# Kernel tuning notes

Hardware: AMD Instinct MI355X
Metric: run time of the kernel (lower is better)

Reference implementation:

```python
import jax, jax.numpy as jnp
import numpy as np

NIN, NHID, NDECHID, NOUT = 128, 256, 512, 10
B, N = 32, 4096


def _linear_params(key, fan_in, fan_out):
    kw, kb = jax.random.split(key)
    bound = 1.0 / np.sqrt(fan_in)
    W = jax.random.uniform(kw, (fan_in, fan_out), jnp.float32, -bound, bound)
    b = jax.random.uniform(kb, (fan_out,), jnp.float32, -bound, bound)
    return W, b


def setup_inputs() -> dict:
    key = jax.random.key(0)
    ks = jax.random.split(key, 7)
    x = jax.random.normal(ks[0], (B, N, NIN), jnp.float32)
    W1, b1 = _linear_params(ks[1], NIN, NHID)
    W2, b2 = _linear_params(ks[2], NHID, NHID)
    W3, b3 = _linear_params(ks[3], NHID, NHID)
    D1, c1 = _linear_params(ks[4], NHID, NDECHID)
    D2, c2 = _linear_params(ks[5], NDECHID, NDECHID)
    D3, c3 = _linear_params(ks[6], NDECHID, NOUT)
    return {"x": x, "W1": W1, "b1": b1, "W2": W2, "b2": b2, "W3": W3, "b3": b3,
            "D1": D1, "c1": c1, "D2": D2, "c2": c2, "D3": D3, "c3": c3}


def reference(x, W1, b1, W2, b2, W3, b3, D1, c1, D2, c2, D3, c3):
    # encoder MLP: Linear-ReLU-Linear-ReLU-Linear, then extra ReLU
    h = jax.nn.relu(x @ W1 + b1)            # [B, N, nhid]
    h = jax.nn.relu(h @ W2 + b2)
    h = jax.nn.relu(h @ W3 + b3)            # fused enc output + F.relu
    # mean_{i,j}(h_i * h_j) over the set == (mean_i h)^2 elementwise (exact identity)
    m = jnp.mean(h, axis=1)                  # [B, nhid]
    p = jax.nn.relu(m * m)                   # [B, nhid]
    # decoder MLP
    d = jax.nn.relu(p @ D1 + c1)
    d = jax.nn.relu(d @ D2 + c2)
    return d @ D3 + c3                       # [B, nout]
```

## Files before the change

### kernel.cpp

```cpp
#include <hip/hip_runtime.h>
#include <hip/hip_bf16.h>
#include <stdint.h>


#define NIN   128
#define NHID  256
#define NDEC  512
#define NOUTC 10
#define BATCH 32
#define NTOK  4096
#define MTILE 64
#define NBLK  (BATCH * (NTOK / MTILE))

#define SWZ(t) (((t) & 7) << 4)

typedef short bf16x8 __attribute__((ext_vector_type(8)));
typedef float floatx4 __attribute__((ext_vector_type(4)));

__device__ __forceinline__ uint16_t f2b(float f) {
  union { uint32_t u; float f; } v; v.f = f;
  uint32_t r = v.u + 0x7FFFu + ((v.u >> 16) & 1u);
  return (uint16_t)(r >> 16);
}
__device__ __forceinline__ uint32_t pkbf(float lo, float hi) {
  __hip_bfloat162 h = __float22bfloat162_rn(float2{lo, hi});
  union { __hip_bfloat162 h; uint32_t u; } c; c.h = h;
  return c.u;
}

__global__ __launch_bounds__(256) void pack_weights(
    const float* __restrict__ W1, const float* __restrict__ W2,
    const float* __restrict__ W3, const float* __restrict__ c3,
    uint8_t* __restrict__ pW, float* __restrict__ msum,
    float* __restrict__ out) {
  int p = blockIdx.x * blockDim.x + threadIdx.x;
  if (p < BATCH * NHID) msum[p] = 0.f;
  if (p < BATCH * NOUTC) out[p] = c3[p % NOUTC];
  if (p < 32768) {
    int j = p & 7, ln = (p >> 3) & 63, rest = p >> 9;
    int kc = rest & 3, mt = rest >> 2;
    int m = mt * 16 + (ln & 15);
    int k = kc * 32 + ((ln >> 4) << 3) + j;
    ((uint16_t*)pW)[p] = f2b(W1[k * NHID + m]);
  } else {
    int p2 = p - 32768;
    const float* W = (p2 < 65536) ? W2 : W3;
    int base = (p2 < 65536) ? 65536 : 131072;
    if (p2 >= 65536) p2 -= 65536;
    int j = p2 & 7, ln = (p2 >> 3) & 63, rest = p2 >> 9;
    int kc = rest & 7, mt = rest >> 3;
    int m = mt * 16 + (ln & 15);
    int k = kc * 32 + ((ln >> 4) << 3) + j;
    int r = __builtin_amdgcn_cvt_pk_fp8_f32(W[k * NHID + m], 0.f, 0, false);
    pW[base + p2] = (uint8_t)(r & 0xFF);
  }
}

__global__ __launch_bounds__(256) void encoder(
    const float* __restrict__ x,
    const uint8_t* __restrict__ pW,
    const float* __restrict__ b1,
    const float* __restrict__ b2,
    const float* __restrict__ b3,
    float* __restrict__ msum) {
  __shared__ __align__(16) uint8_t Hs[MTILE * 256];

  const int tid  = threadIdx.x;
  const int wave = tid >> 6;
  const int lane = tid & 63;
  const int l15  = lane & 15;
  const int q    = lane >> 4;
  const int tok0  = blockIdx.x * MTILE;
  const int batch = blockIdx.x >> 6;

  const uint16_t* pW1 = (const uint16_t*)pW;
  const uint8_t*  pW2 = pW + 65536;
  const uint8_t*  pW3 = pW + 131072;

  {
    const float4* xv = (const float4*)(x + (size_t)tok0 * NIN);
#pragma unroll
    for (int i = 0; i < 4; ++i) {
      const int u = tid + i * 256;
      float4 va = xv[2 * u];
      float4 vb = xv[2 * u + 1];
      uint4 w = make_uint4(pkbf(va.x, va.y), pkbf(va.z, va.w),
                           pkbf(vb.x, vb.y), pkbf(vb.z, vb.w));
      const int row = u >> 4;
      const int cb  = (u & 15) << 4;
      *(uint4*)&Hs[row * 256 + (cb ^ SWZ(row))] = w;
    }
  }
  __syncthreads();

  floatx4 acc[4][4];

#pragma unroll
  for (int jt = 0; jt < 4; ++jt) {
    const float4 bb = *(const float4*)&b1[wave * 64 + jt * 16 + q * 4];
#pragma unroll
    for (int tt = 0; tt < 4; ++tt)
      acc[jt][tt] = (floatx4){bb.x, bb.y, bb.z, bb.w};
  }
#pragma unroll
  for (int kc = 0; kc < 4; ++kc) {
    bf16x8 a[4], b[4];
#pragma unroll
    for (int jt = 0; jt < 4; ++jt)
      a[jt] = *(const bf16x8*)(pW1 + ((((wave * 4 + jt) * 4 + kc) * 64 + lane) << 3));
#pragma unroll
    for (int tt = 0; tt < 4; ++tt) {
      const int t = tt * 16 + l15;
      b[tt] = *(const bf16x8*)&Hs[t * 256 + ((kc * 64 + q * 16) ^ SWZ(t))];
    }
#pragma unroll
    for (int jt = 0; jt < 4; ++jt)
#pragma unroll
      for (int tt = 0; tt < 4; ++tt)
        acc[jt][tt] = __builtin_amdgcn_mfma_f32_16x16x32_bf16(
            a[jt], b[tt], acc[jt][tt], 0, 0, 0);
  }
  __syncthreads();

#pragma unroll
  for (int jt = 0; jt < 4; ++jt) {
    const int j0 = wave * 64 + jt * 16 + q * 4;
#pragma unroll
    for (int tt = 0; tt < 4; ++tt) {
      const int t = tt * 16 + l15;
      float v0 = fmaxf(acc[jt][tt][0], 0.f);
      float v1 = fmaxf(acc[jt][tt][1], 0.f);
      float v2 = fmaxf(acc[jt][tt][2], 0.f);
      float v3 = fmaxf(acc[jt][tt][3], 0.f);
      int u = __builtin_amdgcn_cvt_pk_fp8_f32(v0, v1, 0, false);
      u = __builtin_amdgcn_cvt_pk_fp8_f32(v2, v3, u, true);
      *(uint32_t*)&Hs[t * 256 + (j0 ^ SWZ(t))] = (uint32_t)u;
    }
  }
  __syncthreads();

#pragma unroll
  for (int jt = 0; jt < 4; ++jt) {
    const float4 bb = *(const float4*)&b2[wave * 64 + jt * 16 + q * 4];
#pragma unroll
    for (int tt = 0; tt < 4; ++tt)
      acc[jt][tt] = (floatx4){bb.x, bb.y, bb.z, bb.w};
  }
#pragma unroll
  for (int kc = 0; kc < 8; ++kc) {
    long a[4], b[4];
#pragma unroll
    for (int jt = 0; jt < 4; ++jt)
      a[jt] = *(const long*)(pW2 + ((((wave * 4 + jt) * 8 + kc) * 64 + lane) << 3));
#pragma unroll
    for (int tt = 0; tt < 4; ++tt) {
      const int t = tt * 16 + l15;
      b[tt] = *(const long*)&Hs[t * 256 + ((kc * 32 + q * 8) ^ SWZ(t))];
    }
#pragma unroll
    for (int jt = 0; jt < 4; ++jt)
#pragma unroll
      for (int tt = 0; tt < 4; ++tt)
        acc[jt][tt] = __builtin_amdgcn_mfma_f32_16x16x32_fp8_fp8(
            a[jt], b[tt], acc[jt][tt], 0, 0, 0);
  }
  __syncthreads();

#pragma unroll
  for (int jt = 0; jt < 4; ++jt) {
    const int j0 = wave * 64 + jt * 16 + q * 4;
#pragma unroll
    for (int tt = 0; tt < 4; ++tt) {
      const int t = tt * 16 + l15;
      float v0 = fmaxf(acc[jt][tt][0], 0.f);
      float v1 = fmaxf(acc[jt][tt][1], 0.f);
      float v2 = fmaxf(acc[jt][tt][2], 0.f);
      float v3 = fmaxf(acc[jt][tt][3], 0.f);
      int u = __builtin_amdgcn_cvt_pk_fp8_f32(v0, v1, 0, false);
      u = __builtin_amdgcn_cvt_pk_fp8_f32(v2, v3, u, true);
      *(uint32_t*)&Hs[t * 256 + (j0 ^ SWZ(t))] = (uint32_t)u;
    }
  }
  __syncthreads();

#pragma unroll
  for (int jt = 0; jt < 4; ++jt) {
    const float4 bb = *(const float4*)&b3[wave * 64 + jt * 16 + q * 4];
#pragma unroll
    for (int tt = 0; tt < 4; ++tt)
      acc[jt][tt] = (floatx4){bb.x, bb.y, bb.z, bb.w};
  }
#pragma unroll
  for (int kc = 0; kc < 8; ++kc) {
    long a[4], b[4];
#pragma unroll
    for (int jt = 0; jt < 4; ++jt)
      a[jt] = *(const long*)(pW3 + ((((wave * 4 + jt) * 8 + kc) * 64 + lane) << 3));
#pragma unroll
    for (int tt = 0; tt < 4; ++tt) {
      const int t = tt * 16 + l15;
      b[tt] = *(const long*)&Hs[t * 256 + ((kc * 32 + q * 8) ^ SWZ(t))];
    }
#pragma unroll
    for (int jt = 0; jt < 4; ++jt)
#pragma unroll
      for (int tt = 0; tt < 4; ++tt)
        acc[jt][tt] = __builtin_amdgcn_mfma_f32_16x16x32_fp8_fp8(
            a[jt], b[tt], acc[jt][tt], 0, 0, 0);
  }
#pragma unroll
  for (int jt = 0; jt < 4; ++jt) {
    float s0 = 0.f, s1 = 0.f, s2 = 0.f, s3 = 0.f;
#pragma unroll
    for (int tt = 0; tt < 4; ++tt) {
      s0 += fmaxf(acc[jt][tt][0], 0.f);
      s1 += fmaxf(acc[jt][tt][1], 0.f);
      s2 += fmaxf(acc[jt][tt][2], 0.f);
      s3 += fmaxf(acc[jt][tt][3], 0.f);
    }
#pragma unroll
    for (int m = 1; m <= 8; m <<= 1) {
      s0 += __shfl_xor(s0, m);
      s1 += __shfl_xor(s1, m);
      s2 += __shfl_xor(s2, m);
      s3 += __shfl_xor(s3, m);
    }
    if (l15 == 0) {
      const int jb = batch * NHID + wave * 64 + jt * 16 + q * 4;
      atomicAdd(&msum[jb + 0], s0);
      atomicAdd(&msum[jb + 1], s1);
      atomicAdd(&msum[jb + 2], s2);
      atomicAdd(&msum[jb + 3], s3);
    }
  }
}

__global__ __launch_bounds__(1024) void decoder(
    const float* __restrict__ msum,
    const float* __restrict__ D1, const float* __restrict__ c1,
    const float* __restrict__ D2, const float* __restrict__ c2,
    const float* __restrict__ D3,
    float* __restrict__ out) {
  __shared__ float p[NHID];
  __shared__ float d1[NDEC];
  __shared__ float d2q[128];
  __shared__ __align__(16) float red[4096];
  const int b = blockIdx.x >> 2, qd = blockIdx.x & 3, t = threadIdx.x;

  if (t < NHID) {
    float m = msum[b * NHID + t] * (1.f / NTOK);
    p[t] = m * m;
  }
  __syncthreads();

  {
    const int jg = t & 127;
    const int ks = t >> 7;
    const float4* D1v = (const float4*)D1;
    float4 s = {0.f, 0.f, 0.f, 0.f};
    for (int k = ks * 32; k < ks * 32 + 32; ++k) {
      float4 w = D1v[k * 128 + jg];
      float pv = p[k];
      s.x += pv * w.x; s.y += pv * w.y; s.z += pv * w.z; s.w += pv * w.w;
    }
    *(float4*)&red[t * 4] = s;
    __syncthreads();
    if (t < NDEC) {
      float v = c1[t];
#pragma unroll
      for (int i = 0; i < 8; ++i) v += red[i * 512 + t];
      d1[t] = fmaxf(v, 0.f);
    }
    __syncthreads();
  }

  {
    const int jg2 = t & 31;
    const int ks2 = t >> 5;
    const float4* D2v = (const float4*)D2;
    float4 s = {0.f, 0.f, 0.f, 0.f};
    for (int k = ks2 * 16; k < ks2 * 16 + 16; ++k) {
      float4 w = D2v[k * 128 + qd * 32 + jg2];
      float hv = d1[k];
      s.x += hv * w.x; s.y += hv * w.y; s.z += hv * w.z; s.w += hv * w.w;
    }
    *(float4*)&red[t * 4] = s;
    __syncthreads();
    if (t < 128) {
      float v = c2[qd * 128 + t];
#pragma unroll
      for (int i = 0; i < 32; ++i) v += red[i * 128 + t];
      d2q[t] = fmaxf(v, 0.f);
    }
    __syncthreads();
  }

  {
    const int j3 = t & 15;
    const int kc = t >> 4;
    float s = 0.f;
    if (j3 < NOUTC)
      for (int k = kc * 2; k < kc * 2 + 2; ++k)
        s += d2q[k] * D3[(qd * 128 + k) * NOUTC + j3];
    red[t] = s;
    __syncthreads();
    if (t < NOUTC) {
      float v = 0.f;
#pragma unroll
      for (int i = 0; i < 64; ++i) v += red[i * 16 + t];
      atomicAdd(&out[b * NOUTC + t], v);
    }
  }
}

extern "C" void kernel_launch(void* const* d_in, const int* in_sizes, int n_in,
                              void* d_out, int out_size, void* d_ws, size_t ws_size,
                              hipStream_t stream) {
  const float* x  = (const float*)d_in[0];
  const float* W1 = (const float*)d_in[1];
  const float* b1 = (const float*)d_in[2];
  const float* W2 = (const float*)d_in[3];
  const float* b2 = (const float*)d_in[4];
  const float* W3 = (const float*)d_in[5];
  const float* b3 = (const float*)d_in[6];
  const float* D1 = (const float*)d_in[7];
  const float* c1 = (const float*)d_in[8];
  const float* D2 = (const float*)d_in[9];
  const float* c2 = (const float*)d_in[10];
  const float* D3 = (const float*)d_in[11];
  const float* c3 = (const float*)d_in[12];

  uint8_t* pW   = (uint8_t*)d_ws;
  float*   msum = (float*)((char*)d_ws + 384 * 1024);

  pack_weights<<<640, 256, 0, stream>>>(W1, W2, W3, c3, pW, msum,
                                        (float*)d_out);
  encoder<<<NBLK, 256, 0, stream>>>(x, pW, b1, b2, b3, msum);
  decoder<<<128, 1024, 0, stream>>>(msum, D1, c1, D2, c2, D3,
                                    (float*)d_out);
}
```

Before: 171.2 us.

## Split encoder tile across eight waves and stage per-block sums in LDS

The encoder block grows from 4 to 8 waves. Each wave now owns 32 output features (2 column tiles) instead of 64, which halves the accumulator registers per thread and lets more waves be resident (launch bounds 512, 8). The final per-feature sums go into a shared scratch array, and then 256 threads each issue one atomic, replacing the scattered per-lane atomics. The cost is that each B fragment read from LDS is reused by only 2 A tiles instead of 4, which raises LDS traffic per MFMA, and there is one extra barrier.

Measured after the change: 177.2 us. 1.04x slower.

```diff
diff --git a/kernel.cpp b/kernel.cpp
--- a/kernel.cpp
+++ b/kernel.cpp
@@ -56,7 +56,7 @@
   }
 }
 
-__global__ __launch_bounds__(256) void encoder(
+__global__ __launch_bounds__(512, 8) void encoder(
     const float* __restrict__ x,
     const uint8_t* __restrict__ pW,
     const float* __restrict__ b1,
@@ -64,6 +64,7 @@
     const float* __restrict__ b3,
     float* __restrict__ msum) {
   __shared__ __align__(16) uint8_t Hs[MTILE * 256];
+  __shared__ __align__(16) float scr[NHID];
 
   const int tid  = threadIdx.x;
   const int wave = tid >> 6;
@@ -80,8 +81,8 @@
   {
     const float4* xv = (const float4*)(x + (size_t)tok0 * NIN);
 #pragma unroll
-    for (int i = 0; i < 4; ++i) {
-      const int u = tid + i * 256;
+    for (int i = 0; i < 2; ++i) {
+      const int u = tid + i * 512;
       float4 va = xv[2 * u];
       float4 vb = xv[2 * u + 1];
       uint4 w = make_uint4(pkbf(va.x, va.y), pkbf(va.z, va.w),
@@ -93,38 +94,32 @@
   }
   __syncthreads();
 
-  floatx4 acc[4][4];
-
-#pragma unroll
-  for (int jt = 0; jt < 4; ++jt) {
-    const float4 bb = *(const float4*)&b1[wave * 64 + jt * 16 + q * 4];
+  floatx4 acc[2][4];
+
+#pragma unroll
+  for (int jt = 0; jt < 2; ++jt) {
+    const float4 bb = *(const float4*)&b1[(wave * 2 + jt) * 16 + q * 4];
 #pragma unroll
     for (int tt = 0; tt < 4; ++tt)
       acc[jt][tt] = (floatx4){bb.x, bb.y, bb.z, bb.w};
   }
 #pragma unroll
   for (int kc = 0; kc < 4; ++kc) {
-    bf16x8 a[4], b[4];
-#pragma unroll
-    for (int jt = 0; jt < 4; ++jt)
-      a[jt] = *(const bf16x8*)(pW1 + ((((wave * 4 + jt) * 4 + kc) * 64 + lane) << 3));
-#pragma unroll
-    for (int tt = 0; tt < 4; ++tt) {
-      const int t = tt * 16 + l15;
-      b[tt] = *(const bf16x8*)&Hs[t * 256 + ((kc * 64 + q * 16) ^ SWZ(t))];
-    }
-#pragma unroll
-    for (int jt = 0; jt < 4; ++jt)
-#pragma unroll
-      for (int tt = 0; tt < 4; ++tt)
-        acc[jt][tt] = __builtin_amdgcn_mfma_f32_16x16x32_bf16(
-            a[jt], b[tt], acc[jt][tt], 0, 0, 0);
-  }
-  __syncthreads();
-
-#pragma unroll
-  for (int jt = 0; jt < 4; ++jt) {
-    const int j0 = wave * 64 + jt * 16 + q * 4;
+    bf16x8 a0 = *(const bf16x8*)(pW1 + ((((wave * 2 + 0) * 4 + kc) * 64 + lane) << 3));
+    bf16x8 a1 = *(const bf16x8*)(pW1 + ((((wave * 2 + 1) * 4 + kc) * 64 + lane) << 3));
+#pragma unroll
+    for (int tt = 0; tt < 4; ++tt) {
+      const int t = tt * 16 + l15;
+      bf16x8 b = *(const bf16x8*)&Hs[t * 256 + ((kc * 64 + q * 16) ^ SWZ(t))];
+      acc[0][tt] = __builtin_amdgcn_mfma_f32_16x16x32_bf16(a0, b, acc[0][tt], 0, 0, 0);
+      acc[1][tt] = __builtin_amdgcn_mfma_f32_16x16x32_bf16(a1, b, acc[1][tt], 0, 0, 0);
+    }
+  }
+  __syncthreads();
+
+#pragma unroll
+  for (int jt = 0; jt < 2; ++jt) {
+    const int j0 = (wave * 2 + jt) * 16 + q * 4;
 #pragma unroll
     for (int tt = 0; tt < 4; ++tt) {
       const int t = tt * 16 + l15;
@@ -140,35 +135,29 @@
   __syncthreads();
 
 #pragma unroll
-  for (int jt = 0; jt < 4; ++jt) {
-    const float4 bb = *(const float4*)&b2[wave * 64 + jt * 16 + q * 4];
+  for (int jt = 0; jt < 2; ++jt) {
+    const float4 bb = *(const float4*)&b2[(wave * 2 + jt) * 16 + q * 4];
 #pragma unroll
     for (int tt = 0; tt < 4; ++tt)
       acc[jt][tt] = (floatx4){bb.x, bb.y, bb.z, bb.w};
   }
 #pragma unroll
   for (int kc = 0; kc < 8; ++kc) {
-    long a[4], b[4];
-#pragma unroll
-    for (int jt = 0; jt < 4; ++jt)
-      a[jt] = *(const long*)(pW2 + ((((wave * 4 + jt) * 8 + kc) * 64 + lane) << 3));
-#pragma unroll
-    for (int tt = 0; tt < 4; ++tt) {
-      const int t = tt * 16 + l15;
-      b[tt] = *(const long*)&Hs[t * 256 + ((kc * 32 + q * 8) ^ SWZ(t))];
-    }
-#pragma unroll
-    for (int jt = 0; jt < 4; ++jt)
-#pragma unroll
-      for (int tt = 0; tt < 4; ++tt)
-        acc[jt][tt] = __builtin_amdgcn_mfma_f32_16x16x32_fp8_fp8(
-            a[jt], b[tt], acc[jt][tt], 0, 0, 0);
-  }
-  __syncthreads();
-
-#pragma unroll
-  for (int jt = 0; jt < 4; ++jt) {
-    const int j0 = wave * 64 + jt * 16 + q * 4;
+    long a0 = *(const long*)(pW2 + ((((wave * 2 + 0) * 8 + kc) * 64 + lane) << 3));
+    long a1 = *(const long*)(pW2 + ((((wave * 2 + 1) * 8 + kc) * 64 + lane) << 3));
+#pragma unroll
+    for (int tt = 0; tt < 4; ++tt) {
+      const int t = tt * 16 + l15;
+      long b = *(const long*)&Hs[t * 256 + ((kc * 32 + q * 8) ^ SWZ(t))];
+      acc[0][tt] = __builtin_amdgcn_mfma_f32_16x16x32_fp8_fp8(a0, b, acc[0][tt], 0, 0, 0);
+      acc[1][tt] = __builtin_amdgcn_mfma_f32_16x16x32_fp8_fp8(a1, b, acc[1][tt], 0, 0, 0);
+    }
+  }
+  __syncthreads();
+
+#pragma unroll
+  for (int jt = 0; jt < 2; ++jt) {
+    const int j0 = (wave * 2 + jt) * 16 + q * 4;
 #pragma unroll
     for (int tt = 0; tt < 4; ++tt) {
       const int t = tt * 16 + l15;
@@ -184,32 +173,27 @@
   __syncthreads();
 
 #pragma unroll
-  for (int jt = 0; jt < 4; ++jt) {
-    const float4 bb = *(const float4*)&b3[wave * 64 + jt * 16 + q * 4];
+  for (int jt = 0; jt < 2; ++jt) {
+    const float4 bb = *(const float4*)&b3[(wave * 2 + jt) * 16 + q * 4];
 #pragma unroll
     for (int tt = 0; tt < 4; ++tt)
       acc[jt][tt] = (floatx4){bb.x, bb.y, bb.z, bb.w};
   }
 #pragma unroll
   for (int kc = 0; kc < 8; ++kc) {
-    long a[4], b[4];
-#pragma unroll
-    for (int jt = 0; jt < 4; ++jt)
-      a[jt] = *(const long*)(pW3 + ((((wave * 4 + jt) * 8 + kc) * 64 + lane) << 3));
-#pragma unroll
-    for (int tt = 0; tt < 4; ++tt) {
-      const int t = tt * 16 + l15;
-      b[tt] = *(const long*)&Hs[t * 256 + ((kc * 32 + q * 8) ^ SWZ(t))];
-    }
-#pragma unroll
-    for (int jt = 0; jt < 4; ++jt)
-#pragma unroll
-      for (int tt = 0; tt < 4; ++tt)
-        acc[jt][tt] = __builtin_amdgcn_mfma_f32_16x16x32_fp8_fp8(
-            a[jt], b[tt], acc[jt][tt], 0, 0, 0);
-  }
-#pragma unroll
-  for (int jt = 0; jt < 4; ++jt) {
+    long a0 = *(const long*)(pW3 + ((((wave * 2 + 0) * 8 + kc) * 64 + lane) << 3));
+    long a1 = *(const long*)(pW3 + ((((wave * 2 + 1) * 8 + kc) * 64 + lane) << 3));
+#pragma unroll
+    for (int tt = 0; tt < 4; ++tt) {
+      const int t = tt * 16 + l15;
+      long b = *(const long*)&Hs[t * 256 + ((kc * 32 + q * 8) ^ SWZ(t))];
+      acc[0][tt] = __builtin_amdgcn_mfma_f32_16x16x32_fp8_fp8(a0, b, acc[0][tt], 0, 0, 0);
+      acc[1][tt] = __builtin_amdgcn_mfma_f32_16x16x32_fp8_fp8(a1, b, acc[1][tt], 0, 0, 0);
+    }
+  }
+
+#pragma unroll
+  for (int jt = 0; jt < 2; ++jt) {
     float s0 = 0.f, s1 = 0.f, s2 = 0.f, s3 = 0.f;
 #pragma unroll
     for (int tt = 0; tt < 4; ++tt) {
@@ -225,14 +209,12 @@
       s2 += __shfl_xor(s2, m);
       s3 += __shfl_xor(s3, m);
     }
-    if (l15 == 0) {
-      const int jb = batch * NHID + wave * 64 + jt * 16 + q * 4;
-      atomicAdd(&msum[jb + 0], s0);
-      atomicAdd(&msum[jb + 1], s1);
-      atomicAdd(&msum[jb + 2], s2);
-      atomicAdd(&msum[jb + 3], s3);
-    }
-  }
+    if (l15 == 0)
+      *(float4*)&scr[(wave * 2 + jt) * 16 + q * 4] = (float4){s0, s1, s2, s3};
+  }
+  __syncthreads();
+  if (tid < NHID)
+    atomicAdd(&msum[batch * NHID + tid], scr[tid]);
 }
 
 __global__ __launch_bounds__(1024) void decoder(
@@ -335,7 +317,7 @@
 
   pack_weights<<<640, 256, 0, stream>>>(W1, W2, W3, c3, pW, msum,
                                         (float*)d_out);
-  encoder<<<NBLK, 256, 0, stream>>>(x, pW, b1, b2, b3, msum);
+  encoder<<<NBLK, 512, 0, stream>>>(x, pW, b1, b2, b3, msum);
   decoder<<<128, 1024, 0, stream>>>(msum, D1, c1, D2, c2, D3,
                                     (float*)d_out);
 }
```
